# Kernel tuning notes

Hardware: AMD Instinct MI355X
Metric: run time of the kernel (lower is better)

## Reference

```python
import jax, jax.numpy as jnp
import numpy as np

N = 50000; E = 800000; F_IN = 512; H = 2; C1 = 128; C2 = 32; N_CLASS = 32; N_HID = 64
LOSS_WEIGHT = 0.5


def _layer_norm(x, g, b):
    m = x.mean(-1, keepdims=True)
    v = ((x - m) ** 2).mean(-1, keepdims=True)
    return (x - m) / jnp.sqrt(v + 1e-5) * g + b


def _gat_conv(x, src, dst, n, W, Wh1, bh1, Wh2, bh2, heads, c, concat):
    # x: [n, in]; src/dst: [E'] (self loops already appended)
    xt = (x @ W).reshape(n, heads, c)            # [n, H, C]
    xj = xt[src]                                  # [E', H, C] gathered source feats
    # scaled dot-product attention logits per edge/head
    e = jnp.einsum('ehc,ehc->eh', xt[dst], xj) / np.float32(np.sqrt(c))
    m = jax.ops.segment_max(e, dst, num_segments=n)
    ex = jnp.exp(e - m[dst])
    s = jax.ops.segment_sum(ex, dst, num_segments=n)
    alpha = ex / (s[dst] + 1e-16)                 # [E', H]
    out = jax.ops.segment_sum(alpha[:, :, None] * xj, dst, num_segments=n)  # [n, H, C]
    # per-head auxiliary class prediction head h (DeepGAT)
    h = jax.nn.elu(jnp.einsum('nhc,cd->nhd', xt, Wh1) + bh1)
    h = jnp.einsum('nhd,dk->nhk', h, Wh2) + bh2   # [n, H, n_class]
    out = out.reshape(n, heads * c) if concat else out.mean(axis=1)
    return out, h, alpha


def setup_inputs() -> dict:
    key = jax.random.key(0)
    ks = jax.random.split(key, 24)
    g = lambda k, shape, fan: jax.random.normal(k, shape, jnp.float32) / np.float32(np.sqrt(fan))
    d = {}
    d['x'] = jax.random.normal(ks[0], (N, F_IN), jnp.float32)
    d['edge_index'] = jax.random.randint(ks[1], (2, E), 0, N, jnp.int32)
    # layer 1: F_IN -> H*C1 (concat)
    d['W1'] = g(ks[2], (F_IN, H * C1), F_IN)
    d['Wh1a'] = g(ks[3], (C1, N_HID), C1); d['bh1a'] = jnp.zeros((N_HID,), jnp.float32)
    d['Wh2a'] = g(ks[4], (N_HID, N_CLASS), N_HID); d['bh2a'] = jnp.zeros((N_CLASS,), jnp.float32)
    d['g1'] = jnp.ones((H * C1,), jnp.float32); d['b1'] = jnp.zeros((H * C1,), jnp.float32)
    # layer 2: H*C1 -> H*C2 (concat)
    d['W2'] = g(ks[5], (H * C1, H * C2), H * C1)
    d['Wh1b'] = g(ks[6], (C2, N_HID), C2); d['bh1b'] = jnp.zeros((N_HID,), jnp.float32)
    d['Wh2b'] = g(ks[7], (N_HID, N_CLASS), N_HID); d['bh2b'] = jnp.zeros((N_CLASS,), jnp.float32)
    d['g2'] = jnp.ones((H * C2,), jnp.float32); d['b2'] = jnp.zeros((H * C2,), jnp.float32)
    # layer 3: H*C2 -> N_CLASS (mean over heads)
    d['W3'] = g(ks[8], (H * C2, H * N_CLASS), H * C2)
    d['Wh1c'] = g(ks[9], (N_CLASS, N_HID), N_CLASS); d['bh1c'] = jnp.zeros((N_HID,), jnp.float32)
    d['Wh2c'] = g(ks[10], (N_HID, N_CLASS), N_HID); d['bh2c'] = jnp.zeros((N_CLASS,), jnp.float32)
    d['g3'] = jnp.ones((N_CLASS,), jnp.float32); d['b3'] = jnp.zeros((N_CLASS,), jnp.float32)
    return d


def reference(x, edge_index, W1, Wh1a, bh1a, Wh2a, bh2a, g1, b1,
              W2, Wh1b, bh1b, Wh2b, bh2b, g2, b2,
              W3, Wh1c, bh1c, Wh2c, bh2c, g3, b3):
    n = x.shape[0]
    loops = jnp.arange(n, dtype=edge_index.dtype)
    src = jnp.concatenate([edge_index[0], loops])
    dst = jnp.concatenate([edge_index[1], loops])
    # eval mode: F.dropout is identity
    x1, h1, _ = _gat_conv(x, src, dst, n, W1, Wh1a, bh1a, Wh2a, bh2a, H, C1, True)
    x1 = jax.nn.elu(_layer_norm(x1, g1, b1))
    x2, h2, _ = _gat_conv(x1, src, dst, n, W2, Wh1b, bh1b, Wh2b, bh2b, H, C2, True)
    x2 = jax.nn.elu(_layer_norm(x2, g2, b2))
    x3, h3, alpha = _gat_conv(x2, src, dst, n, W3, Wh1c, bh1c, Wh2c, bh2c, H, N_CLASS, False)
    x3 = _layer_norm(x3, g3, b3)
    return (x3, h1, h2 * LOSS_WEIGHT, h3, alpha)
```

## Files before the change

### kernel.cpp

```cpp
#include <hip/hip_runtime.h>

#define NN 50000
#define EE 800000
#define EPN 850000

typedef __attribute__((ext_vector_type(8))) short bf16x8;
typedef __attribute__((ext_vector_type(4))) float f32x4;
typedef unsigned short ushort_t;

__device__ __forceinline__ float eluf(float v) { return v > 0.f ? v : expm1f(v); }
__device__ __forceinline__ unsigned short f2bf(float f) {
  unsigned u = __float_as_uint(f);
  unsigned r = (u + 0x7FFFu + ((u >> 16) & 1u)) >> 16;
  return (unsigned short)r;
}
__device__ __forceinline__ float bf2f(unsigned short b) {
  return __uint_as_float(((unsigned)b) << 16);
}
__device__ __forceinline__ void unpack8(uint4 u, float* o) {
  o[0] = __uint_as_float(u.x << 16); o[1] = __uint_as_float(u.x & 0xFFFF0000u);
  o[2] = __uint_as_float(u.y << 16); o[3] = __uint_as_float(u.y & 0xFFFF0000u);
  o[4] = __uint_as_float(u.z << 16); o[5] = __uint_as_float(u.z & 0xFFFF0000u);
  o[6] = __uint_as_float(u.w << 16); o[7] = __uint_as_float(u.w & 0xFFFF0000u);
}
__device__ __forceinline__ void gload_lds16(const ushort_t* g, ushort_t* l) {
  __builtin_amdgcn_global_load_lds((const __attribute__((address_space(1))) void*)g,
                                   (__attribute__((address_space(3))) void*)l, 16, 0, 0);
}

__global__ __launch_bounds__(256) void conv_w1(const float* __restrict__ W,
                                               ushort_t* __restrict__ Wc) {
  int idx = blockIdx.x * 256 + threadIdx.x;
  if (idx >= 256 * 1024) return;
  int col = idx >> 10, rem = idx & 1023;
  int kb = rem >> 6, j = rem & 63;
  int sel = j >> 5, k = j & 31;
  int gk = kb * 32 + k;
  float v = W[(size_t)gk * 256 + col];
  unsigned short h = f2bf(v);
  Wc[idx] = sel ? (ushort_t)f2bf(v - bf2f(h)) : h;
}

__global__ __launch_bounds__(256) void gemm1_mfma(const float* __restrict__ A,
                                                  const ushort_t* __restrict__ Wc,
                                                  ushort_t* __restrict__ C16, int M) {
  constexpr int K = 512;
  __shared__ alignas(16) ushort_t Bs[2][128 * 64];
  int tid = threadIdx.x;
  int w = tid >> 6, lane = tid & 63, l15 = lane & 15, l4 = lane >> 4;
  int row0 = blockIdx.y * 64, col0 = blockIdx.x * 128;
  int arow = row0 + w * 16 + l15;
  int arowc = arow < M ? arow : M - 1;
  const float* arp = A + (size_t)arowc * K + l4 * 8;

  int chunk_src = (lane & 7) ^ ((lane >> 3) & 7);
  const ushort_t* wsrc =
      Wc + (size_t)(col0 + w * 32 + (lane >> 3)) * 1024 + chunk_src * 8;
  ushort_t* ldst0 = &Bs[0][(w * 32) * 64];
  ushort_t* ldst1 = &Bs[1][(w * 32) * 64];

  int swz = l15 & 7;
  int roff_h = ((l4 ^ swz) << 3);
  int roff_l = (((l4 | 4) ^ swz) << 3);
  int rbase = l15 * 64;

  f32x4 acc[8];
#pragma unroll
  for (int t = 0; t < 8; ++t) acc[t] = (f32x4){0.f, 0.f, 0.f, 0.f};

#pragma unroll
  for (int q = 0; q < 4; ++q) gload_lds16(wsrc + q * 8192, ldst0 + q * 512);
  float4 pa0c = *(const float4*)(arp);
  float4 pa1c = *(const float4*)(arp + 4);
  float4 pa0n, pa1n;

  for (int k0 = 0; k0 < K; k0 += 32) {
    int kb = k0 >> 5, p = kb & 1;
    __syncthreads();
    if (k0 + 32 < K) {
      ushort_t* dst = (p ? ldst0 : ldst1);
      const ushort_t* src = wsrc + (kb + 1) * 64;
#pragma unroll
      for (int q = 0; q < 4; ++q) gload_lds16(src + q * 8192, dst + q * 512);
      pa0n = *(const float4*)(arp + k0 + 32);
      pa1n = *(const float4*)(arp + k0 + 36);
    }
    bf16x8 ah, al;
    {
      float v[8] = {pa0c.x, pa0c.y, pa0c.z, pa0c.w, pa1c.x, pa1c.y, pa1c.z, pa1c.w};
#pragma unroll
      for (int i = 0; i < 8; ++i) {
        unsigned short h = f2bf(v[i]);
        ah[i] = (short)h;
        al[i] = (short)f2bf(v[i] - bf2f(h));
      }
    }
    const ushort_t* bp = &Bs[p][rbase];
#pragma unroll
    for (int t = 0; t < 8; ++t) {
      bf16x8 b_h = *(const bf16x8*)&bp[t * 1024 + roff_h];
      bf16x8 b_l = *(const bf16x8*)&bp[t * 1024 + roff_l];
      acc[t] = __builtin_amdgcn_mfma_f32_16x16x32_bf16(ah, b_h, acc[t], 0, 0, 0);
      acc[t] = __builtin_amdgcn_mfma_f32_16x16x32_bf16(ah, b_l, acc[t], 0, 0, 0);
      acc[t] = __builtin_amdgcn_mfma_f32_16x16x32_bf16(al, b_h, acc[t], 0, 0, 0);
    }
    pa0c = pa0n; pa1c = pa1n;
  }
#pragma unroll
  for (int t = 0; t < 8; ++t) {
#pragma unroll
    for (int r = 0; r < 4; ++r) {
      int grow = row0 + w * 16 + l4 * 4 + r;
      if (grow < M) C16[(size_t)grow * 256 + col0 + t * 16 + l15] = f2bf(acc[t][r]);
    }
  }
}

template <int NT>
__global__ __launch_bounds__(256) void gemm_mfma(const float* __restrict__ A,
                                                 const float* __restrict__ B,
                                                 ushort_t* __restrict__ C16,
                                                 int M, int N, int K) {
  __shared__ unsigned short Ah[64 * 40], Al[64 * 40];
  __shared__ unsigned short Bh[NT * 16 * 40], Bl[NT * 16 * 40];
  int tid = threadIdx.x;
  int wave = tid >> 6, lane = tid & 63;
  int l15 = lane & 15, l4 = lane >> 4;
  int row0 = blockIdx.y * 64, col0 = blockIdx.x * (NT * 16);

  f32x4 acc[NT];
#pragma unroll
  for (int t = 0; t < NT; ++t) acc[t] = (f32x4){0.f, 0.f, 0.f, 0.f};

  int ar = tid >> 2;
  int ak = (tid & 3) * 8;
  constexpr int TPC = 256 / (NT * 16);
  constexpr int NK = 32 / TPC;
  int bc = tid / TPC;
  int bk = (tid % TPC) * NK;

  for (int k0 = 0; k0 < K; k0 += 32) {
    {
      float v[8];
      int grow = row0 + ar;
      if (grow < M) {
        float4 q0 = *(const float4*)&A[(size_t)grow * K + k0 + ak];
        float4 q1 = *(const float4*)&A[(size_t)grow * K + k0 + ak + 4];
        v[0] = q0.x; v[1] = q0.y; v[2] = q0.z; v[3] = q0.w;
        v[4] = q1.x; v[5] = q1.y; v[6] = q1.z; v[7] = q1.w;
      } else {
#pragma unroll
        for (int i = 0; i < 8; ++i) v[i] = 0.f;
      }
      bf16x8 hv, lv;
#pragma unroll
      for (int i = 0; i < 8; ++i) {
        unsigned short h = f2bf(v[i]);
        hv[i] = (short)h;
        lv[i] = (short)f2bf(v[i] - bf2f(h));
      }
      *(bf16x8*)&Ah[ar * 40 + ak] = hv;
      *(bf16x8*)&Al[ar * 40 + ak] = lv;
    }
    {
#pragma unroll
      for (int i = 0; i < NK; ++i) {
        float v = B[(size_t)(k0 + bk + i) * N + col0 + bc];
        unsigned short h = f2bf(v);
        Bh[bc * 40 + bk + i] = h;
        Bl[bc * 40 + bk + i] = f2bf(v - bf2f(h));
      }
    }
    __syncthreads();
    bf16x8 a_h = *(const bf16x8*)&Ah[(wave * 16 + l15) * 40 + l4 * 8];
    bf16x8 a_l = *(const bf16x8*)&Al[(wave * 16 + l15) * 40 + l4 * 8];
#pragma unroll
    for (int t = 0; t < NT; ++t) {
      bf16x8 b_h = *(const bf16x8*)&Bh[(t * 16 + l15) * 40 + l4 * 8];
      bf16x8 b_l = *(const bf16x8*)&Bl[(t * 16 + l15) * 40 + l4 * 8];
      acc[t] = __builtin_amdgcn_mfma_f32_16x16x32_bf16(a_h, b_h, acc[t], 0, 0, 0);
      acc[t] = __builtin_amdgcn_mfma_f32_16x16x32_bf16(a_h, b_l, acc[t], 0, 0, 0);
      acc[t] = __builtin_amdgcn_mfma_f32_16x16x32_bf16(a_l, b_h, acc[t], 0, 0, 0);
    }
    __syncthreads();
  }
#pragma unroll
  for (int t = 0; t < NT; ++t) {
#pragma unroll
    for (int r = 0; r < 4; ++r) {
      int grow = row0 + wave * 16 + l4 * 4 + r;
      if (grow < M) C16[(size_t)grow * N + col0 + t * 16 + l15] = f2bf(acc[t][r]);
    }
  }
}

template <int C>
__global__ __launch_bounds__(256) void aux_mfma(const ushort_t* __restrict__ xt16,
                                                const float* __restrict__ Wh1,
                                                const float* __restrict__ bh1,
                                                const float* __restrict__ Wh2,
                                                const float* __restrict__ bh2,
                                                float* __restrict__ hout,
                                                float scale) {
  constexpr int KS = C / 32;
  constexpr int LDB = C + 8;
  __shared__ unsigned short BhS[64 * LDB], BlS[64 * LDB];
  __shared__ float w2s[64 * 32];
  __shared__ float hid[64 * 68];
  int tid = threadIdx.x;
  for (int i = tid; i < C * 64; i += 256) {
    int k = i >> 6, col = i & 63;
    float v = Wh1[i];
    unsigned short h = f2bf(v);
    BhS[col * LDB + k] = h;
    BlS[col * LDB + k] = f2bf(v - bf2f(h));
  }
  for (int i = tid; i < 64 * 32; i += 256) w2s[i] = Wh2[i];
  __syncthreads();

  int w = tid >> 6, lane = tid & 63, l15 = lane & 15, l4 = lane >> 4;
  int gr = blockIdx.x * 64 + w * 16 + l15;
  const int M2 = 2 * NN;

  f32x4 acc[4];
#pragma unroll
  for (int t = 0; t < 4; ++t) acc[t] = (f32x4){0.f, 0.f, 0.f, 0.f};

#pragma unroll
  for (int ks = 0; ks < KS; ++ks) {
    bf16x8 ah;
    if (gr < M2) {
      ah = *(const bf16x8*)(xt16 + (size_t)gr * C + ks * 32 + l4 * 8);
    } else {
      ah = (bf16x8){0, 0, 0, 0, 0, 0, 0, 0};
    }
#pragma unroll
    for (int t = 0; t < 4; ++t) {
      bf16x8 b_h = *(const bf16x8*)&BhS[(t * 16 + l15) * LDB + ks * 32 + l4 * 8];
      bf16x8 b_l = *(const bf16x8*)&BlS[(t * 16 + l15) * LDB + ks * 32 + l4 * 8];
      acc[t] = __builtin_amdgcn_mfma_f32_16x16x32_bf16(ah, b_h, acc[t], 0, 0, 0);
      acc[t] = __builtin_amdgcn_mfma_f32_16x16x32_bf16(ah, b_l, acc[t], 0, 0, 0);
    }
  }
#pragma unroll
  for (int t = 0; t < 4; ++t) {
    float bb = bh1[t * 16 + l15];
#pragma unroll
    for (int r = 0; r < 4; ++r)
      hid[(w * 16 + l4 * 4 + r) * 68 + t * 16 + l15] = eluf(acc[t][r] + bb);
  }
  __syncthreads();
  float4 o0 = make_float4(0.f, 0.f, 0.f, 0.f), o1 = o0;
  const float* hrow = &hid[(w * 16 + l15) * 68];
#pragma unroll 8
  for (int k = 0; k < 64; ++k) {
    float hv = hrow[k];
    float4 wa = *(const float4*)&w2s[k * 32 + l4 * 8];
    float4 wb = *(const float4*)&w2s[k * 32 + l4 * 8 + 4];
    o0.x += hv * wa.x; o0.y += hv * wa.y; o0.z += hv * wa.z; o0.w += hv * wa.w;
    o1.x += hv * wb.x; o1.y += hv * wb.y; o1.z += hv * wb.z; o1.w += hv * wb.w;
  }
  if (gr < M2) {
    float4 ba = *(const float4*)&bh2[l4 * 8];
    float4 bb = *(const float4*)&bh2[l4 * 8 + 4];
    o0.x = (o0.x + ba.x) * scale; o0.y = (o0.y + ba.y) * scale;
    o0.z = (o0.z + ba.z) * scale; o0.w = (o0.w + ba.w) * scale;
    o1.x = (o1.x + bb.x) * scale; o1.y = (o1.y + bb.y) * scale;
    o1.z = (o1.z + bb.z) * scale; o1.w = (o1.w + bb.w) * scale;
    float* dst = hout + (size_t)(gr >> 1) * 64 + (gr & 1) * 32 + l4 * 8;
    *(float4*)dst = o0;
    *(float4*)(dst + 4) = o1;
  }
}

__global__ __launch_bounds__(256) void hist_kernel(const int* __restrict__ ei,
                                                   int* __restrict__ cnt) {
  int e = blockIdx.x * 256 + threadIdx.x;
  if (e >= EPN) return;
  int d = (e < EE) ? ei[EE + e] : e - EE;
  atomicAdd(&cnt[d], 1);
}

__global__ __launch_bounds__(1024) void scan_blocks(const int* __restrict__ cnt,
                                                    int* __restrict__ tmp,
                                                    int* __restrict__ bsum) {
  __shared__ int lds[1024];
  int t = threadIdx.x, idx = blockIdx.x * 1024 + t;
  int v = (idx < NN) ? cnt[idx] : 0;
  lds[t] = v;
  __syncthreads();
  for (int off = 1; off < 1024; off <<= 1) {
    int add = (t >= off) ? lds[t - off] : 0;
    __syncthreads();
    lds[t] += add;
    __syncthreads();
  }
  if (idx < NN) tmp[idx] = lds[t];
  if (t == 1023) bsum[blockIdx.x] = lds[t];
}

__global__ __launch_bounds__(64) void scan_bsum(int* __restrict__ bsum, int nb) {
  int t = threadIdx.x;
  int v = (t < nb) ? bsum[t] : 0;
#pragma unroll
  for (int off = 1; off < 64; off <<= 1) {
    int u = __shfl_up(v, off);
    if (t >= off) v += u;
  }
  if (t < nb) bsum[t] = v;
}

__global__ __launch_bounds__(256) void scan_final(const int* __restrict__ cnt,
                                                  const int* __restrict__ tmp,
                                                  const int* __restrict__ bsum,
                                                  int* __restrict__ rowptr,
                                                  int* __restrict__ fill) {
  int idx = blockIdx.x * 256 + threadIdx.x;
  if (idx >= NN) return;
  int b = idx >> 10;
  int off = (b > 0) ? bsum[b - 1] : 0;
  int inc = tmp[idx] + off;
  rowptr[idx + 1] = inc;
  fill[idx] = inc - cnt[idx];
  if (idx == 0) rowptr[0] = 0;
}

__global__ __launch_bounds__(256) void scatter_kernel(const int* __restrict__ ei,
                                                      int* __restrict__ fill,
                                                      int* __restrict__ eids,
                                                      int* __restrict__ srcs) {
  int e = blockIdx.x * 256 + threadIdx.x;
  if (e >= EPN) return;
  int d, s;
  if (e < EE) { d = ei[EE + e]; s = ei[e]; } else { d = s = e - EE; }
  int pos = atomicAdd(&fill[d], 1);
  eids[pos] = e;
  srcs[pos] = s;
}

__global__ __launch_bounds__(256) void gat256_fused(const ushort_t* __restrict__ xt16,
                                                    const int* __restrict__ srcs,
                                                    const int* __restrict__ rowptr,
                                                    float* __restrict__ outb,
                                                    const float* __restrict__ g,
                                                    const float* __restrict__ b) {
  int node = (int)((blockIdx.x * (size_t)blockDim.x + threadIdx.x) >> 6);
  int lane = threadIdx.x & 63;
  if (node >= NN) return;
  int start = rowptr[node], end = rowptr[node + 1];
  float4 dstv;
  {
    uint2 u = ((const uint2*)(xt16 + (size_t)node * 256))[lane];
    dstv.x = __uint_as_float(u.x << 16);
    dstv.y = __uint_as_float(u.x & 0xFFFF0000u);
    dstv.z = __uint_as_float(u.y << 16);
    dstv.w = __uint_as_float(u.y & 0xFFFF0000u);
  }
  float m = -3e38f, s = 0.f;
  float4 acc = make_float4(0.f, 0.f, 0.f, 0.f);
  int i = start;
  for (; i + 8 <= end; i += 8) {
    int sj[8];
    float4 a[8];
    float p[8];
#pragma unroll
    for (int j = 0; j < 8; ++j) sj[j] = srcs[i + j];
#pragma unroll
    for (int j = 0; j < 8; ++j) {
      uint2 u = ((const uint2*)(xt16 + (size_t)sj[j] * 256))[lane];
      a[j].x = __uint_as_float(u.x << 16);
      a[j].y = __uint_as_float(u.x & 0xFFFF0000u);
      a[j].z = __uint_as_float(u.y << 16);
      a[j].w = __uint_as_float(u.y & 0xFFFF0000u);
    }
#pragma unroll
    for (int j = 0; j < 8; ++j) {
      float p_ = a[j].x * dstv.x + a[j].y * dstv.y + a[j].z * dstv.z + a[j].w * dstv.w;
      p_ += __shfl_xor(p_, 1); p_ += __shfl_xor(p_, 2); p_ += __shfl_xor(p_, 4);
      p_ += __shfl_xor(p_, 8); p_ += __shfl_xor(p_, 16);
      p[j] = p_ * 0.08838834764831843f;
    }
    float pm = p[0];
#pragma unroll
    for (int j = 1; j < 8; ++j) pm = fmaxf(pm, p[j]);
    if (__any(pm > m + 8.f)) {
#pragma unroll
      for (int j = 0; j < 8; ++j) {
        float mn = fmaxf(m, p[j]);
        float scf = __expf(m - mn), w = __expf(p[j] - mn);
        s = s * scf + w;
        acc.x = acc.x * scf + w * a[j].x;
        acc.y = acc.y * scf + w * a[j].y;
        acc.z = acc.z * scf + w * a[j].z;
        acc.w = acc.w * scf + w * a[j].w;
        m = mn;
      }
    } else {
#pragma unroll
      for (int j = 0; j < 8; ++j) {
        float w = __expf(p[j] - m);
        s += w;
        acc.x = fmaf(w, a[j].x, acc.x);
        acc.y = fmaf(w, a[j].y, acc.y);
        acc.z = fmaf(w, a[j].z, acc.z);
        acc.w = fmaf(w, a[j].w, acc.w);
      }
    }
  }
  for (; i < end; ++i) {
    int s0 = srcs[i];
    float4 a0;
    uint2 u = ((const uint2*)(xt16 + (size_t)s0 * 256))[lane];
    a0.x = __uint_as_float(u.x << 16);
    a0.y = __uint_as_float(u.x & 0xFFFF0000u);
    a0.z = __uint_as_float(u.y << 16);
    a0.w = __uint_as_float(u.y & 0xFFFF0000u);
    float p_ = a0.x * dstv.x + a0.y * dstv.y + a0.z * dstv.z + a0.w * dstv.w;
    p_ += __shfl_xor(p_, 1); p_ += __shfl_xor(p_, 2); p_ += __shfl_xor(p_, 4);
    p_ += __shfl_xor(p_, 8); p_ += __shfl_xor(p_, 16);
    p_ *= 0.08838834764831843f;
    float mn = fmaxf(m, p_);
    float scf = __expf(m - mn), w = __expf(p_ - mn);
    s = s * scf + w;
    acc.x = acc.x * scf + w * a0.x;
    acc.y = acc.y * scf + w * a0.y;
    acc.z = acc.z * scf + w * a0.z;
    acc.w = acc.w * scf + w * a0.w;
    m = mn;
  }
  float inv = 1.f / (s + 1e-16f);
  float4 v;
  v.x = acc.x * inv; v.y = acc.y * inv; v.z = acc.z * inv; v.w = acc.w * inv;
  float sum = v.x + v.y + v.z + v.w;
#pragma unroll
  for (int o = 1; o < 64; o <<= 1) sum += __shfl_xor(sum, o);
  float mean = sum * (1.f / 256.f);
  float dx = v.x - mean, dy = v.y - mean, dz = v.z - mean, dw = v.w - mean;
  float q = dx * dx + dy * dy + dz * dz + dw * dw;
#pragma unroll
  for (int o = 1; o < 64; o <<= 1) q += __shfl_xor(q, o);
  float rstd = rsqrtf(q * (1.f / 256.f) + 1e-5f);
  float4 gg = ((const float4*)g)[lane], bb = ((const float4*)b)[lane];
  float4 r;
  r.x = eluf(dx * rstd * gg.x + bb.x);
  r.y = eluf(dy * rstd * gg.y + bb.y);
  r.z = eluf(dz * rstd * gg.z + bb.z);
  r.w = eluf(dw * rstd * gg.w + bb.w);
  ((float4*)(outb + (size_t)node * 256))[lane] = r;
}

template <int MODE>
__global__ __launch_bounds__(256) void gat64_t(const ushort_t* __restrict__ xt16,
                                               const int* __restrict__ srcs,
                                               const int* __restrict__ eids,
                                               const int* __restrict__ rowptr,
                                               float* __restrict__ outb,
                                               float* __restrict__ logit_out,
                                               float* __restrict__ mbuf,
                                               float* __restrict__ sbuf,
                                               const float* __restrict__ g,
                                               const float* __restrict__ b) {
  int node = (int)((blockIdx.x * (size_t)blockDim.x + threadIdx.x) >> 6);
  int lane = threadIdx.x & 63;
  if (node >= NN) return;
  int l32 = lane & 31, half = lane >> 5;
  int start = rowptr[node], end = rowptr[node + 1];
  float dv[32];
  {
    const ushort_t* dp = xt16 + (size_t)node * 64 + half * 32;
    unpack8(*(const uint4*)(dp), dv);
    unpack8(*(const uint4*)(dp + 8), dv + 8);
    unpack8(*(const uint4*)(dp + 16), dv + 16);
    unpack8(*(const uint4*)(dp + 24), dv + 24);
  }
  float m = -3e38f, s = 0.f, acc = 0.f;

  for (int base = start; base < end; base += 32) {
    int cnt = end - base;
    cnt = cnt > 32 ? 32 : cnt;
    int sidx = srcs[base + (l32 < cnt ? l32 : 0)];
    float sv[32];
    {
      const ushort_t* sp = xt16 + (size_t)sidx * 64 + half * 32;
      unpack8(*(const uint4*)(sp), sv);
      unpack8(*(const uint4*)(sp + 8), sv + 8);
      unpack8(*(const uint4*)(sp + 16), sv + 16);
      unpack8(*(const uint4*)(sp + 24), sv + 24);
    }
    float p = 0.f;
#pragma unroll
    for (int k = 0; k < 32; ++k) p = fmaf(sv[k], dv[k], p);
    p *= 0.17677669529663687f;
    if (MODE == 1) {
      if (l32 < cnt) logit_out[(size_t)eids[base + l32] * 2 + half] = p;
    }
    if (l32 >= cnt) p = -3e38f;
    float bm = p;
    bm = fmaxf(bm, __shfl_xor(bm, 1));
    bm = fmaxf(bm, __shfl_xor(bm, 2));
    bm = fmaxf(bm, __shfl_xor(bm, 4));
    bm = fmaxf(bm, __shfl_xor(bm, 8));
    bm = fmaxf(bm, __shfl_xor(bm, 16));
    float mn = fmaxf(m, bm);
    float scf = __expf(m - mn);
    float w = (l32 < cnt) ? __expf(p - mn) : 0.f;
    float bs = w;
    bs += __shfl_xor(bs, 1);
    bs += __shfl_xor(bs, 2);
    bs += __shfl_xor(bs, 4);
    bs += __shfl_xor(bs, 8);
    bs += __shfl_xor(bs, 16);
    s = s * scf + bs;
    acc *= scf;
    m = mn;
#pragma unroll 4
    for (int e = 0; e < cnt; ++e) {
      int sj = __shfl(sidx, e);
      float wv = __shfl(w, e + (half << 5));
      float a = bf2f(xt16[(size_t)sj * 64 + lane]);
      acc = fmaf(wv, a, acc);
    }
  }
  float inv = 1.f / (s + 1e-16f);
  float v = acc * inv;
  if (MODE == 0) {
    float sum = v;
#pragma unroll
    for (int o = 1; o < 64; o <<= 1) sum += __shfl_xor(sum, o);
    float mean = sum * (1.f / 64.f);
    float dvv = v - mean;
    float q = dvv * dvv;
#pragma unroll
    for (int o = 1; o < 64; o <<= 1) q += __shfl_xor(q, o);
    float rstd = rsqrtf(q * (1.f / 64.f) + 1e-5f);
    outb[(size_t)node * 64 + lane] = eluf(dvv * rstd * g[lane] + b[lane]);
  } else {
    if (l32 == 0) {
      mbuf[(size_t)node * 2 + half] = m;
      sbuf[(size_t)node * 2 + half] = s;
    }
    float t = __shfl_xor(v, 32);
    float y = 0.5f * (v + t);
    float sum = y;
#pragma unroll
    for (int o = 1; o < 32; o <<= 1) sum += __shfl_xor(sum, o);
    float mean = sum * (1.f / 32.f);
    float dy = y - mean;
    float q = dy * dy;
#pragma unroll
    for (int o = 1; o < 32; o <<= 1) q += __shfl_xor(q, o);
    float rstd = rsqrtf(q * (1.f / 32.f) + 1e-5f);
    if (half == 0) outb[(size_t)node * 32 + l32] = dy * rstd * g[l32] + b[l32];
  }
}

__global__ __launch_bounds__(256) void alpha_fix(float* __restrict__ al,
                                                 const int* __restrict__ ei,
                                                 const float* __restrict__ mbuf,
                                                 const float* __restrict__ sbuf) {
  size_t i = blockIdx.x * (size_t)blockDim.x + threadIdx.x;
  if (i >= (size_t)EPN * 2) return;
  int e = (int)(i >> 1), h = (int)(i & 1);
  int d = (e < EE) ? ei[EE + e] : e - EE;
  al[i] = expf(al[i] - mbuf[(size_t)d * 2 + h]) / (sbuf[(size_t)d * 2 + h] + 1e-16f);
}

extern "C" void kernel_launch(void* const* d_in, const int* in_sizes, int n_in,
                              void* d_out, int out_size, void* d_ws, size_t ws_size,
                              hipStream_t stream) {
  const float* x    = (const float*)d_in[0];
  const int*   ei   = (const int*)d_in[1];
  const float* W1   = (const float*)d_in[2];
  const float* Wh1a = (const float*)d_in[3];
  const float* bh1a = (const float*)d_in[4];
  const float* Wh2a = (const float*)d_in[5];
  const float* bh2a = (const float*)d_in[6];
  const float* g1   = (const float*)d_in[7];
  const float* b1   = (const float*)d_in[8];
  const float* W2   = (const float*)d_in[9];
  const float* Wh1b = (const float*)d_in[10];
  const float* bh1b = (const float*)d_in[11];
  const float* Wh2b = (const float*)d_in[12];
  const float* bh2b = (const float*)d_in[13];
  const float* g2   = (const float*)d_in[14];
  const float* b2   = (const float*)d_in[15];
  const float* W3   = (const float*)d_in[16];
  const float* Wh1c = (const float*)d_in[17];
  const float* bh1c = (const float*)d_in[18];
  const float* Wh2c = (const float*)d_in[19];
  const float* bh2c = (const float*)d_in[20];
  const float* g3   = (const float*)d_in[21];
  const float* b3   = (const float*)d_in[22];

  float* out  = (float*)d_out;
  float* o_x3 = out;
  float* o_h1 = out + (size_t)NN * 32;
  float* o_h2 = o_h1 + (size_t)NN * 64;
  float* o_h3 = o_h2 + (size_t)NN * 64;
  float* o_al = o_h3 + (size_t)NN * 64;

  float* ws  = (float*)d_ws;
  float* A   = ws;
  float* Bb  = ws + (size_t)NN * 256;
  int* cnt    = (int*)(Bb + (size_t)NN * 256);
  int* rowptr = cnt + NN;
  int* fill   = rowptr + NN + 1;
  int* eids   = fill + NN;
  int* srcs   = eids + EPN;
  int* tmp    = srcs + EPN;
  int* bsum   = tmp + NN;
  float* mbuf = (float*)(bsum + 64);
  float* sbuf = mbuf + (size_t)NN * 2;
  ushort_t* W1c = (ushort_t*)(sbuf + (size_t)NN * 2);
  ushort_t* A16 = (ushort_t*)A;

  dim3 blk(256);
  int gEdges = (EPN + 255) / 256;
  int gNodeW = (NN * 64 + 255) / 256;
  int gRows = (NN + 63) / 64;
  int gPairs = (int)(((size_t)EPN * 2 + 255) / 256);
  int gAux = (2 * NN + 63) / 64;
  int nbScan = (NN + 1023) / 1024;

  conv_w1<<<1024, blk, 0, stream>>>(W1, W1c);
  hipMemsetAsync(cnt, 0, (size_t)NN * 4, stream);
  hist_kernel<<<gEdges, blk, 0, stream>>>(ei, cnt);
  scan_blocks<<<nbScan, 1024, 0, stream>>>(cnt, tmp, bsum);
  scan_bsum<<<1, 64, 0, stream>>>(bsum, nbScan);
  scan_final<<<(NN + 255) / 256, blk, 0, stream>>>(cnt, tmp, bsum, rowptr, fill);
  scatter_kernel<<<gEdges, blk, 0, stream>>>(ei, fill, eids, srcs);

  gemm1_mfma<<<dim3(2, gRows), blk, 0, stream>>>(x, W1c, A16, NN);
  aux_mfma<128><<<gAux, blk, 0, stream>>>(A16, Wh1a, bh1a, Wh2a, bh2a, o_h1, 1.0f);
  gat256_fused<<<gNodeW, blk, 0, stream>>>(A16, srcs, rowptr, Bb, g1, b1);

  gemm_mfma<4><<<dim3(1, gRows), blk, 0, stream>>>(Bb, W2, A16, NN, 64, 256);
  aux_mfma<32><<<gAux, blk, 0, stream>>>(A16, Wh1b, bh1b, Wh2b, bh2b, o_h2, 0.5f);
  gat64_t<0><<<gNodeW, blk, 0, stream>>>(A16, srcs, nullptr, rowptr, Bb, nullptr,
                                         nullptr, nullptr, g2, b2);

  gemm_mfma<4><<<dim3(1, gRows), blk, 0, stream>>>(Bb, W3, A16, NN, 64, 64);
  aux_mfma<32><<<gAux, blk, 0, stream>>>(A16, Wh1c, bh1c, Wh2c, bh2c, o_h3, 1.0f);
  gat64_t<1><<<gNodeW, blk, 0, stream>>>(A16, srcs, eids, rowptr, o_x3, o_al,
                                         mbuf, sbuf, g3, b3);
  alpha_fix<<<gPairs, blk, 0, stream>>>(o_al, ei, mbuf, sbuf);
}
```

Measured before the change: 534.0 us.

## Use split-bf16 MFMA for aux second layer and split edges across half-waves in gat256

```diff
diff --git a/kernel.cpp b/kernel.cpp
--- a/kernel.cpp
+++ b/kernel.cpp
@@ -204,9 +204,17 @@
                                                 float scale) {
   constexpr int KS = C / 32;
   constexpr int LDB = C + 8;
-  __shared__ unsigned short BhS[64 * LDB], BlS[64 * LDB];
-  __shared__ float w2s[64 * 32];
-  __shared__ float hid[64 * 68];
+  constexpr int UNION_B = 64 * LDB * 2 * 2;
+  constexpr int UNION_H = 64 * 72 * 2 * 2;
+  constexpr int UNION = UNION_B > UNION_H ? UNION_B : UNION_H;
+  __shared__ alignas(16) char smem[9216 + UNION];
+  ushort_t* w2h = (ushort_t*)smem;
+  ushort_t* w2l = w2h + 32 * 72;
+  ushort_t* BhS = (ushort_t*)(smem + 9216);
+  ushort_t* BlS = BhS + 64 * LDB;
+  ushort_t* hidh = (ushort_t*)(smem + 9216);
+  ushort_t* hidl = hidh + 64 * 72;
+
   int tid = threadIdx.x;
   for (int i = tid; i < C * 64; i += 256) {
     int k = i >> 6, col = i & 63;
@@ -215,7 +223,13 @@
     BhS[col * LDB + k] = h;
     BlS[col * LDB + k] = f2bf(v - bf2f(h));
   }
-  for (int i = tid; i < 64 * 32; i += 256) w2s[i] = Wh2[i];
+  for (int i = tid; i < 64 * 32; i += 256) {
+    int k = i >> 5, col = i & 31;
+    float v = Wh2[i];
+    unsigned short h = f2bf(v);
+    w2h[col * 72 + k] = h;
+    w2l[col * 72 + k] = f2bf(v - bf2f(h));
+  }
   __syncthreads();
 
   int w = tid >> 6, lane = tid & 63, l15 = lane & 15, l4 = lane >> 4;
@@ -242,34 +256,46 @@
       acc[t] = __builtin_amdgcn_mfma_f32_16x16x32_bf16(ah, b_l, acc[t], 0, 0, 0);
     }
   }
+  __syncthreads();
 #pragma unroll
   for (int t = 0; t < 4; ++t) {
     float bb = bh1[t * 16 + l15];
 #pragma unroll
-    for (int r = 0; r < 4; ++r)
-      hid[(w * 16 + l4 * 4 + r) * 68 + t * 16 + l15] = eluf(acc[t][r] + bb);
+    for (int r = 0; r < 4; ++r) {
+      float h = eluf(acc[t][r] + bb);
+      unsigned short hh = f2bf(h);
+      int row = w * 16 + l4 * 4 + r, col = t * 16 + l15;
+      hidh[row * 72 + col] = hh;
+      hidl[row * 72 + col] = f2bf(h - bf2f(hh));
+    }
   }
   __syncthreads();
-  float4 o0 = make_float4(0.f, 0.f, 0.f, 0.f), o1 = o0;
-  const float* hrow = &hid[(w * 16 + l15) * 68];
-#pragma unroll 8
-  for (int k = 0; k < 64; ++k) {
-    float hv = hrow[k];
-    float4 wa = *(const float4*)&w2s[k * 32 + l4 * 8];
-    float4 wb = *(const float4*)&w2s[k * 32 + l4 * 8 + 4];
-    o0.x += hv * wa.x; o0.y += hv * wa.y; o0.z += hv * wa.z; o0.w += hv * wa.w;
-    o1.x += hv * wb.x; o1.y += hv * wb.y; o1.z += hv * wb.z; o1.w += hv * wb.w;
-  }
-  if (gr < M2) {
-    float4 ba = *(const float4*)&bh2[l4 * 8];
-    float4 bb = *(const float4*)&bh2[l4 * 8 + 4];
-    o0.x = (o0.x + ba.x) * scale; o0.y = (o0.y + ba.y) * scale;
-    o0.z = (o0.z + ba.z) * scale; o0.w = (o0.w + ba.w) * scale;
-    o1.x = (o1.x + bb.x) * scale; o1.y = (o1.y + bb.y) * scale;
-    o1.z = (o1.z + bb.z) * scale; o1.w = (o1.w + bb.w) * scale;
-    float* dst = hout + (size_t)(gr >> 1) * 64 + (gr & 1) * 32 + l4 * 8;
-    *(float4*)dst = o0;
-    *(float4*)(dst + 4) = o1;
+  f32x4 acc2[2];
+  acc2[0] = (f32x4){0.f, 0.f, 0.f, 0.f};
+  acc2[1] = acc2[0];
+#pragma unroll
+  for (int ks = 0; ks < 2; ++ks) {
+    bf16x8 ah = *(const bf16x8*)&hidh[(w * 16 + l15) * 72 + ks * 32 + l4 * 8];
+    bf16x8 al = *(const bf16x8*)&hidl[(w * 16 + l15) * 72 + ks * 32 + l4 * 8];
+#pragma unroll
+    for (int t2 = 0; t2 < 2; ++t2) {
+      bf16x8 b_h = *(const bf16x8*)&w2h[(t2 * 16 + l15) * 72 + ks * 32 + l4 * 8];
+      bf16x8 b_l = *(const bf16x8*)&w2l[(t2 * 16 + l15) * 72 + ks * 32 + l4 * 8];
+      acc2[t2] = __builtin_amdgcn_mfma_f32_16x16x32_bf16(ah, b_h, acc2[t2], 0, 0, 0);
+      acc2[t2] = __builtin_amdgcn_mfma_f32_16x16x32_bf16(ah, b_l, acc2[t2], 0, 0, 0);
+      acc2[t2] = __builtin_amdgcn_mfma_f32_16x16x32_bf16(al, b_h, acc2[t2], 0, 0, 0);
+    }
+  }
+#pragma unroll
+  for (int t2 = 0; t2 < 2; ++t2) {
+    int col = t2 * 16 + l15;
+    float bb = bh2[col];
+#pragma unroll
+    for (int r = 0; r < 4; ++r) {
+      int gr2 = blockIdx.x * 64 + w * 16 + l4 * 4 + r;
+      if (gr2 < M2)
+        hout[(size_t)(gr2 >> 1) * 64 + (gr2 & 1) * 32 + col] = (acc2[t2][r] + bb) * scale;
+    }
   }
 }
 
@@ -347,106 +373,105 @@
   int node = (int)((blockIdx.x * (size_t)blockDim.x + threadIdx.x) >> 6);
   int lane = threadIdx.x & 63;
   if (node >= NN) return;
+  int l32 = lane & 31, half = lane >> 5;
   int start = rowptr[node], end = rowptr[node + 1];
-  float4 dstv;
-  {
-    uint2 u = ((const uint2*)(xt16 + (size_t)node * 256))[lane];
-    dstv.x = __uint_as_float(u.x << 16);
-    dstv.y = __uint_as_float(u.x & 0xFFFF0000u);
-    dstv.z = __uint_as_float(u.y << 16);
-    dstv.w = __uint_as_float(u.y & 0xFFFF0000u);
-  }
-  float m = -3e38f, s = 0.f;
-  float4 acc = make_float4(0.f, 0.f, 0.f, 0.f);
+  float dv[8];
+  unpack8(*(const uint4*)(xt16 + (size_t)node * 256 + l32 * 8), dv);
+  float m = -3e38f, s_h = 0.f;
+  float acc[8] = {0.f, 0.f, 0.f, 0.f, 0.f, 0.f, 0.f, 0.f};
+
   int i = start;
   for (; i + 8 <= end; i += 8) {
-    int sj[8];
-    float4 a[8];
-    float p[8];
-#pragma unroll
-    for (int j = 0; j < 8; ++j) sj[j] = srcs[i + j];
-#pragma unroll
-    for (int j = 0; j < 8; ++j) {
-      uint2 u = ((const uint2*)(xt16 + (size_t)sj[j] * 256))[lane];
-      a[j].x = __uint_as_float(u.x << 16);
-      a[j].y = __uint_as_float(u.x & 0xFFFF0000u);
-      a[j].z = __uint_as_float(u.y << 16);
-      a[j].w = __uint_as_float(u.y & 0xFFFF0000u);
-    }
-#pragma unroll
-    for (int j = 0; j < 8; ++j) {
-      float p_ = a[j].x * dstv.x + a[j].y * dstv.y + a[j].z * dstv.z + a[j].w * dstv.w;
-      p_ += __shfl_xor(p_, 1); p_ += __shfl_xor(p_, 2); p_ += __shfl_xor(p_, 4);
-      p_ += __shfl_xor(p_, 8); p_ += __shfl_xor(p_, 16);
-      p[j] = p_ * 0.08838834764831843f;
-    }
-    float pm = p[0];
-#pragma unroll
-    for (int j = 1; j < 8; ++j) pm = fmaxf(pm, p[j]);
+    int sj[4];
+    float sv[4][8];
+    float p[4];
+#pragma unroll
+    for (int q = 0; q < 4; ++q) sj[q] = srcs[i + q * 2 + half];
+#pragma unroll
+    for (int q = 0; q < 4; ++q)
+      unpack8(*(const uint4*)(xt16 + (size_t)sj[q] * 256 + l32 * 8), sv[q]);
+#pragma unroll
+    for (int q = 0; q < 4; ++q) {
+      float p_ = 0.f;
+#pragma unroll
+      for (int k = 0; k < 8; ++k) p_ = fmaf(sv[q][k], dv[k], p_);
+      p_ += __shfl_xor(p_, 1); p_ += __shfl_xor(p_, 2);
+      p_ += __shfl_xor(p_, 4); p_ += __shfl_xor(p_, 8);
+      p[q] = p_ * 0.08838834764831843f;
+    }
+    float pm = fmaxf(fmaxf(p[0], p[1]), fmaxf(p[2], p[3]));
     if (__any(pm > m + 8.f)) {
 #pragma unroll
-      for (int j = 0; j < 8; ++j) {
-        float mn = fmaxf(m, p[j]);
-        float scf = __expf(m - mn), w = __expf(p[j] - mn);
-        s = s * scf + w;
-        acc.x = acc.x * scf + w * a[j].x;
-        acc.y = acc.y * scf + w * a[j].y;
-        acc.z = acc.z * scf + w * a[j].z;
-        acc.w = acc.w * scf + w * a[j].w;
+      for (int q = 0; q < 4; ++q) {
+        float pb = fmaxf(p[q], __shfl_xor(p[q], 32));
+        float mn = fmaxf(m, pb);
+        float scf = __expf(m - mn), w = __expf(p[q] - mn);
+        s_h = s_h * scf + w;
+#pragma unroll
+        for (int k = 0; k < 8; ++k) acc[k] = fmaf(w, sv[q][k], acc[k] * scf);
         m = mn;
       }
     } else {
 #pragma unroll
-      for (int j = 0; j < 8; ++j) {
-        float w = __expf(p[j] - m);
-        s += w;
-        acc.x = fmaf(w, a[j].x, acc.x);
-        acc.y = fmaf(w, a[j].y, acc.y);
-        acc.z = fmaf(w, a[j].z, acc.z);
-        acc.w = fmaf(w, a[j].w, acc.w);
+      for (int q = 0; q < 4; ++q) {
+        float w = __expf(p[q] - m);
+        s_h += w;
+#pragma unroll
+        for (int k = 0; k < 8; ++k) acc[k] = fmaf(w, sv[q][k], acc[k]);
       }
     }
   }
-  for (; i < end; ++i) {
-    int s0 = srcs[i];
-    float4 a0;
-    uint2 u = ((const uint2*)(xt16 + (size_t)s0 * 256))[lane];
-    a0.x = __uint_as_float(u.x << 16);
-    a0.y = __uint_as_float(u.x & 0xFFFF0000u);
-    a0.z = __uint_as_float(u.y << 16);
-    a0.w = __uint_as_float(u.y & 0xFFFF0000u);
-    float p_ = a0.x * dstv.x + a0.y * dstv.y + a0.z * dstv.z + a0.w * dstv.w;
-    p_ += __shfl_xor(p_, 1); p_ += __shfl_xor(p_, 2); p_ += __shfl_xor(p_, 4);
-    p_ += __shfl_xor(p_, 8); p_ += __shfl_xor(p_, 16);
+  for (; i < end; i += 2) {
+    bool valid = (i + half) < end;
+    int sj = srcs[valid ? i + half : i];
+    float sv[8];
+    unpack8(*(const uint4*)(xt16 + (size_t)sj * 256 + l32 * 8), sv);
+    float p_ = 0.f;
+#pragma unroll
+    for (int k = 0; k < 8; ++k) p_ = fmaf(sv[k], dv[k], p_);
+    p_ += __shfl_xor(p_, 1); p_ += __shfl_xor(p_, 2);
+    p_ += __shfl_xor(p_, 4); p_ += __shfl_xor(p_, 8);
     p_ *= 0.08838834764831843f;
-    float mn = fmaxf(m, p_);
-    float scf = __expf(m - mn), w = __expf(p_ - mn);
-    s = s * scf + w;
-    acc.x = acc.x * scf + w * a0.x;
-    acc.y = acc.y * scf + w * a0.y;
-    acc.z = acc.z * scf + w * a0.z;
-    acc.w = acc.w * scf + w * a0.w;
+    if (!valid) p_ = -3e38f;
+    float pb = fmaxf(p_, __shfl_xor(p_, 32));
+    float mn = fmaxf(m, pb);
+    float scf = __expf(m - mn);
+    float w = valid ? __expf(p_ - mn) : 0.f;
+    s_h = s_h * scf + w;
+#pragma unroll
+    for (int k = 0; k < 8; ++k) acc[k] = fmaf(w, sv[k], acc[k] * scf);
     m = mn;
   }
+  float s = s_h + __shfl_xor(s_h, 32);
+#pragma unroll
+  for (int k = 0; k < 8; ++k) acc[k] += __shfl_xor(acc[k], 32);
   float inv = 1.f / (s + 1e-16f);
-  float4 v;
-  v.x = acc.x * inv; v.y = acc.y * inv; v.z = acc.z * inv; v.w = acc.w * inv;
-  float sum = v.x + v.y + v.z + v.w;
-#pragma unroll
-  for (int o = 1; o < 64; o <<= 1) sum += __shfl_xor(sum, o);
+  float v[8];
+#pragma unroll
+  for (int k = 0; k < 8; ++k) v[k] = acc[k] * inv;
+  float sum = 0.f;
+#pragma unroll
+  for (int k = 0; k < 8; ++k) sum += v[k];
+  sum += __shfl_xor(sum, 1); sum += __shfl_xor(sum, 2); sum += __shfl_xor(sum, 4);
+  sum += __shfl_xor(sum, 8); sum += __shfl_xor(sum, 16);
   float mean = sum * (1.f / 256.f);
-  float dx = v.x - mean, dy = v.y - mean, dz = v.z - mean, dw = v.w - mean;
-  float q = dx * dx + dy * dy + dz * dz + dw * dw;
-#pragma unroll
-  for (int o = 1; o < 64; o <<= 1) q += __shfl_xor(q, o);
+  float q = 0.f;
+#pragma unroll
+  for (int k = 0; k < 8; ++k) { v[k] -= mean; q = fmaf(v[k], v[k], q); }
+  q += __shfl_xor(q, 1); q += __shfl_xor(q, 2); q += __shfl_xor(q, 4);
+  q += __shfl_xor(q, 8); q += __shfl_xor(q, 16);
   float rstd = rsqrtf(q * (1.f / 256.f) + 1e-5f);
-  float4 gg = ((const float4*)g)[lane], bb = ((const float4*)b)[lane];
-  float4 r;
-  r.x = eluf(dx * rstd * gg.x + bb.x);
-  r.y = eluf(dy * rstd * gg.y + bb.y);
-  r.z = eluf(dz * rstd * gg.z + bb.z);
-  r.w = eluf(dw * rstd * gg.w + bb.w);
-  ((float4*)(outb + (size_t)node * 256))[lane] = r;
+  if (half == 0) {
+    float4 ga = *(const float4*)&g[l32 * 8], gb = *(const float4*)&g[l32 * 8 + 4];
+    float4 ba = *(const float4*)&b[l32 * 8], bb = *(const float4*)&b[l32 * 8 + 4];
+    float4 r0, r1;
+    r0.x = eluf(v[0] * rstd * ga.x + ba.x); r0.y = eluf(v[1] * rstd * ga.y + ba.y);
+    r0.z = eluf(v[2] * rstd * ga.z + ba.z); r0.w = eluf(v[3] * rstd * ga.w + ba.w);
+    r1.x = eluf(v[4] * rstd * gb.x + bb.x); r1.y = eluf(v[5] * rstd * gb.y + bb.y);
+    r1.z = eluf(v[6] * rstd * gb.z + bb.z); r1.w = eluf(v[7] * rstd * gb.w + bb.w);
+    *(float4*)(outb + (size_t)node * 256 + l32 * 8) = r0;
+    *(float4*)(outb + (size_t)node * 256 + l32 * 8 + 4) = r1;
+  }
 }
 
 template <int MODE>
@@ -454,7 +479,7 @@
                                                const int* __restrict__ srcs,
                                                const int* __restrict__ eids,
                                                const int* __restrict__ rowptr,
-                                               float* __restrict__ outb,
+                                               float* __restrict__ outf,
                                                float* __restrict__ logit_out,
                                                float* __restrict__ mbuf,
                                                float* __restrict__ sbuf,
@@ -533,7 +558,7 @@
 #pragma unroll
     for (int o = 1; o < 64; o <<= 1) q += __shfl_xor(q, o);
     float rstd = rsqrtf(q * (1.f / 64.f) + 1e-5f);
-    outb[(size_t)node * 64 + lane] = eluf(dvv * rstd * g[lane] + b[lane]);
+    outf[(size_t)node * 64 + lane] = eluf(dvv * rstd * g[lane] + b[lane]);
   } else {
     if (l32 == 0) {
       mbuf[(size_t)node * 2 + half] = m;
@@ -550,7 +575,7 @@
 #pragma unroll
     for (int o = 1; o < 32; o <<= 1) q += __shfl_xor(q, o);
     float rstd = rsqrtf(q * (1.f / 32.f) + 1e-5f);
-    if (half == 0) outb[(size_t)node * 32 + l32] = dy * rstd * g[l32] + b[l32];
+    if (half == 0) outf[(size_t)node * 32 + l32] = dy * rstd * g[l32] + b[l32];
   }
 }
 
```

New measurement: 515.3 us. 3.5% less time.
